# Kernel tuning notes

Measured on AMD Instinct MI355X. Metric: run time of the kernel, lower is better.

## Reference

```python
import jax, jax.numpy as jnp
import numpy as np

D_MODEL = 1024
NUM_HEADS = 16
HEAD_DIM = D_MODEL // NUM_HEADS
D_FF = 4 * D_MODEL


def _linear_params(key, d_in, d_out):
    kw, kb = jax.random.split(key)
    bound = 1.0 / np.sqrt(d_in)
    W = jax.random.uniform(kw, (d_in, d_out), minval=-bound, maxval=bound, dtype=jnp.float32)
    b = jax.random.uniform(kb, (d_out,), minval=-bound, maxval=bound, dtype=jnp.float32)
    return W, b


def setup_inputs() -> dict:
    key = jax.random.key(0)
    ks = jax.random.split(key, 6)
    x = jax.random.normal(ks[0], (4, 2048, D_MODEL), dtype=jnp.float32)
    qkv_w, qkv_b = _linear_params(ks[1], D_MODEL, 3 * D_MODEL)
    out_w, out_b = _linear_params(ks[2], D_MODEL, D_MODEL)
    ffn1_w, ffn1_b = _linear_params(ks[3], D_MODEL, D_FF)
    ffn2_w, ffn2_b = _linear_params(ks[4], D_FF, D_MODEL)
    ln1_g = jnp.ones((D_MODEL,), jnp.float32); ln1_b = jnp.zeros((D_MODEL,), jnp.float32)
    ln2_g = jnp.ones((D_MODEL,), jnp.float32); ln2_b = jnp.zeros((D_MODEL,), jnp.float32)
    return {
        "x": x,
        "qkv_w": qkv_w, "qkv_b": qkv_b,
        "out_w": out_w, "out_b": out_b,
        "ffn1_w": ffn1_w, "ffn1_b": ffn1_b,
        "ffn2_w": ffn2_w, "ffn2_b": ffn2_b,
        "ln1_g": ln1_g, "ln1_b": ln1_b,
        "ln2_g": ln2_g, "ln2_b": ln2_b,
    }


def _layer_norm(x, g, b, eps=1e-5):
    mu = jnp.mean(x, axis=-1, keepdims=True)
    var = jnp.mean(jnp.square(x - mu), axis=-1, keepdims=True)
    return (x - mu) * jax.lax.rsqrt(var + eps) * g + b


def reference(x, qkv_w, qkv_b, out_w, out_b, ffn1_w, ffn1_b, ffn2_w, ffn2_b,
              ln1_g, ln1_b, ln2_g, ln2_b):
    B, S, D = x.shape
    H, Hd = NUM_HEADS, HEAD_DIM
    normed = _layer_norm(x, ln1_g, ln1_b)
    qkv = normed @ qkv_w + qkv_b                      # [B,S,3D]
    qkv = qkv.reshape(B, S, 3, H, Hd)
    q = jnp.transpose(qkv[:, :, 0], (0, 2, 1, 3))     # [B,H,S,Hd]
    k = jnp.transpose(qkv[:, :, 1], (0, 2, 1, 3))
    v = jnp.transpose(qkv[:, :, 2], (0, 2, 1, 3))
    scores = jnp.einsum('bhqd,bhkd->bhqk', q, k) / np.sqrt(Hd).astype(np.float32)
    causal = jnp.tril(jnp.ones((S, S), dtype=bool))
    scores = jnp.where(causal[None, None], scores, -jnp.inf)
    attn = jax.nn.softmax(scores, axis=-1)
    attn_out = jnp.einsum('bhqk,bhkd->bhqd', attn, v)  # [B,H,S,Hd]
    attn_out = jnp.transpose(attn_out, (0, 2, 1, 3)).reshape(B, S, D)
    attn_out = attn_out @ out_w + out_b
    x = x + attn_out
    h = _layer_norm(x, ln2_g, ln2_b)
    h = jax.nn.gelu(h @ ffn1_w + ffn1_b, approximate=False)
    h = h @ ffn2_w + ffn2_b
    return x + h
```

## Files before the change

### kernel.cpp

```cpp
#include <hip/hip_runtime.h>
#include <hip/hip_bf16.h>
#include <math.h>

typedef __attribute__((ext_vector_type(8))) short short8;
typedef __attribute__((ext_vector_type(4))) float f32x4;

__device__ __forceinline__ float bf2f(unsigned short u) {
    union { unsigned int i; float f; } c; c.i = ((unsigned int)u) << 16; return c.f;
}
__device__ __forceinline__ unsigned short f2bf(float f) {
    union { float f; unsigned int i; } c; c.f = f;
    unsigned int i = c.i;
    unsigned int r = (i + 0x7FFFu + ((i >> 16) & 1u)) >> 16;
    return (unsigned short)r;
}
__device__ __forceinline__ float fexp2(float x) { return __builtin_amdgcn_exp2f(x); }

__device__ __forceinline__ void load8(const unsigned short* p, float* v) {
    short8 s = *(const short8*)p;
#pragma unroll
    for (int i = 0; i < 8; i++) v[i] = bf2f((unsigned short)s[i]);
}
__device__ __forceinline__ void load8(const float* p, float* v) {
    f32x4 a = ((const f32x4*)p)[0], b = ((const f32x4*)p)[1];
    v[0] = a[0]; v[1] = a[1]; v[2] = a[2]; v[3] = a[3];
    v[4] = b[0]; v[5] = b[1]; v[6] = b[2]; v[7] = b[3];
}
__device__ __forceinline__ void store8(unsigned short* p, const float* v) {
    short8 s;
#pragma unroll
    for (int i = 0; i < 8; i++) s[i] = (short)f2bf(v[i]);
    *(short8*)p = s;
}
__device__ __forceinline__ void store8(float* p, const float* v) {
    f32x4 a, b;
    a[0] = v[0]; a[1] = v[1]; a[2] = v[2]; a[3] = v[3];
    b[0] = v[4]; b[1] = v[5]; b[2] = v[6]; b[3] = v[7];
    ((f32x4*)p)[0] = a; ((f32x4*)p)[1] = b;
}

__global__ __launch_bounds__(256) void ln_f32_kernel(
    const float* __restrict__ x, const float* __restrict__ g,
    const float* __restrict__ b, unsigned short* __restrict__ out) {
    const int row = blockIdx.x;
    const int t = threadIdx.x;
    const float* xr = x + (size_t)row * 1024;
    float4 raw = ((const float4*)xr)[t];
    float v0 = raw.x, v1 = raw.y, v2 = raw.z, v3 = raw.w;
    float s = v0 + v1 + v2 + v3;
    float ss = v0 * v0 + v1 * v1 + v2 * v2 + v3 * v3;
    for (int off = 32; off > 0; off >>= 1) {
        s += __shfl_down(s, off);
        ss += __shfl_down(ss, off);
    }
    __shared__ float red[8];
    __shared__ float stat[2];
    const int wave = t >> 6, lane = t & 63;
    if (lane == 0) { red[wave] = s; red[4 + wave] = ss; }
    __syncthreads();
    if (t == 0) {
        float st = red[0] + red[1] + red[2] + red[3];
        float sst = red[4] + red[5] + red[6] + red[7];
        float mu = st * (1.0f / 1024.0f);
        float var = sst * (1.0f / 1024.0f) - mu * mu;
        stat[0] = mu; stat[1] = rsqrtf(var + 1e-5f);
    }
    __syncthreads();
    const float mu = stat[0], rstd = stat[1];
    float4 gr = ((const float4*)g)[t];
    float4 br = ((const float4*)b)[t];
    ushort4 o;
    o.x = f2bf((v0 - mu) * rstd * gr.x + br.x);
    o.y = f2bf((v1 - mu) * rstd * gr.y + br.y);
    o.z = f2bf((v2 - mu) * rstd * gr.z + br.z);
    o.w = f2bf((v3 - mu) * rstd * gr.w + br.w);
    ((ushort4*)(out + (size_t)row * 1024))[t] = o;
}

__global__ __launch_bounds__(256) void ln_bf16_kernel(
    const unsigned short* __restrict__ x, const float* __restrict__ g,
    const float* __restrict__ b, unsigned short* __restrict__ out) {
    const int row = blockIdx.x;
    const int t = threadIdx.x;
    const unsigned short* xr = x + (size_t)row * 1024;
    ushort4 raw = ((const ushort4*)xr)[t];
    float v0 = bf2f(raw.x), v1 = bf2f(raw.y), v2 = bf2f(raw.z), v3 = bf2f(raw.w);
    float s = v0 + v1 + v2 + v3;
    float ss = v0 * v0 + v1 * v1 + v2 * v2 + v3 * v3;
    for (int off = 32; off > 0; off >>= 1) {
        s += __shfl_down(s, off);
        ss += __shfl_down(ss, off);
    }
    __shared__ float red[8];
    __shared__ float stat[2];
    const int wave = t >> 6, lane = t & 63;
    if (lane == 0) { red[wave] = s; red[4 + wave] = ss; }
    __syncthreads();
    if (t == 0) {
        float st = red[0] + red[1] + red[2] + red[3];
        float sst = red[4] + red[5] + red[6] + red[7];
        float mu = st * (1.0f / 1024.0f);
        float var = sst * (1.0f / 1024.0f) - mu * mu;
        stat[0] = mu; stat[1] = rsqrtf(var + 1e-5f);
    }
    __syncthreads();
    const float mu = stat[0], rstd = stat[1];
    float4 gr = ((const float4*)g)[t];
    float4 br = ((const float4*)b)[t];
    ushort4 o;
    o.x = f2bf((v0 - mu) * rstd * gr.x + br.x);
    o.y = f2bf((v1 - mu) * rstd * gr.y + br.y);
    o.z = f2bf((v2 - mu) * rstd * gr.z + br.z);
    o.w = f2bf((v3 - mu) * rstd * gr.w + br.w);
    ((ushort4*)(out + (size_t)row * 1024))[t] = o;
}

__global__ __launch_bounds__(256) void transpose_cast_kernel(
    const float* __restrict__ in, unsigned short* __restrict__ out, int R, int C) {
    __shared__ unsigned short tile[32][33];
    const int bx = blockIdx.x * 32, by = blockIdx.y * 32;
    const int tx = threadIdx.x & 31, ty = threadIdx.x >> 5;
    for (int i = 0; i < 32; i += 8)
        tile[ty + i][tx] = f2bf(in[(size_t)(by + ty + i) * C + bx + tx]);
    __syncthreads();
    for (int i = 0; i < 32; i += 8)
        out[(size_t)(bx + ty + i) * R + by + tx] = tile[tx][ty + i];
}

enum { EPI_QKV = 0, EPI_RES = 1, EPI_GELU = 2 };

template <int EPI, typename RT, typename OT>
__global__ __launch_bounds__(256) void gemm_bt(
    const unsigned short* __restrict__ A, const unsigned short* __restrict__ Bt,
    const float* __restrict__ bias, const RT* __restrict__ res,
    OT* __restrict__ o0, unsigned short* __restrict__ o1,
    unsigned short* __restrict__ o2, int M, int N, int K) {
    constexpr int LDW = 40;
    constexpr int LE = 136;
    __shared__ __align__(16) unsigned short SMEM[20480];
    const int t = threadIdx.x;
    const int wave = t >> 6, lane = t & 63;
    const int lr = lane & 15, lq = lane >> 4;
    const int wm = (wave >> 1) * 64, wn = (wave & 1) * 64;
    const int m0 = blockIdx.y * 128, n0 = blockIdx.x * 128;
    f32x4 acc[4][4] = {};
    const int arow = t >> 2, acol = (t & 3) << 3;
    const unsigned short* ag = A + (size_t)(m0 + arow) * K + acol;
    const unsigned short* bg = Bt + (size_t)(n0 + arow) * K + acol;
    const size_t rstride = (size_t)64 * K;
    short8 a0 = *(const short8*)(ag);
    short8 a1 = *(const short8*)(ag + rstride);
    short8 b0 = *(const short8*)(bg);
    short8 b1 = *(const short8*)(bg + rstride);
    const int nit = K >> 5;
    for (int it = 0; it < nit; ++it) {
        const int buf = (it & 1) * 10240;
        unsigned short* As = SMEM + buf;
        unsigned short* Bs = SMEM + buf + 5120;
        *(short8*)(As + arow * LDW + acol) = a0;
        *(short8*)(As + (arow + 64) * LDW + acol) = a1;
        *(short8*)(Bs + arow * LDW + acol) = b0;
        *(short8*)(Bs + (arow + 64) * LDW + acol) = b1;
        if (it + 1 < nit) {
            const int k0 = (it + 1) << 5;
            a0 = *(const short8*)(ag + k0);
            a1 = *(const short8*)(ag + rstride + k0);
            b0 = *(const short8*)(bg + k0);
            b1 = *(const short8*)(bg + rstride + k0);
        }
        __syncthreads();
        short8 af[4], bfr[4];
#pragma unroll
        for (int i = 0; i < 4; i++) af[i] = *(const short8*)(As + (wm + i * 16 + lr) * LDW + lq * 8);
#pragma unroll
        for (int i = 0; i < 4; i++) bfr[i] = *(const short8*)(Bs + (wn + i * 16 + lr) * LDW + lq * 8);
#pragma unroll
        for (int mi = 0; mi < 4; mi++)
#pragma unroll
            for (int ni = 0; ni < 4; ni++)
                acc[mi][ni] = __builtin_amdgcn_mfma_f32_16x16x32_bf16(af[mi], bfr[ni], acc[mi][ni], 0, 0, 0);
    }
    __syncthreads();
    const bool vreg = (EPI == EPI_QKV) && (n0 >= 2048);
#pragma unroll
    for (int ni = 0; ni < 4; ni++) {
        const int col = wn + ni * 16 + lr;
        const float bv = bias[n0 + col];
#pragma unroll
        for (int mi = 0; mi < 4; mi++) {
#pragma unroll
            for (int r = 0; r < 4; r++) {
                const int row = wm + mi * 16 + lq * 4 + r;
                float val = acc[mi][ni][r] + bv;
                if (EPI == EPI_GELU)
                    val = 0.5f * val * (1.0f + erff(val * 0.70710678118654752f));
                if (vreg) SMEM[col * LE + row] = f2bf(val);
                else      SMEM[row * LE + col] = f2bf(val);
            }
        }
    }
    __syncthreads();
    const int rr = t >> 1, half = (t & 1) * 64;
    if (EPI == EPI_RES || EPI == EPI_GELU) {
        const size_t base = (size_t)(m0 + rr) * N + n0 + half;
        const unsigned short* src = SMEM + rr * LE + half;
#pragma unroll
        for (int j = 0; j < 8; j++) {
            float v[8];
            load8(src + j * 8, v);
            if (EPI == EPI_RES) {
                float rv[8];
                load8(res + base + j * 8, rv);
#pragma unroll
                for (int i = 0; i < 8; i++) v[i] += rv[i];
            }
            store8(o0 + base + j * 8, v);
        }
    } else if (!vreg) {
        const int gcol0 = n0 + half;
        const int which = gcol0 >> 10;
        const int hn = (gcol0 & 1023) >> 6;
        const int grow = m0 + rr;
        const size_t bh = (size_t)((grow >> 11) * 16 + hn);
        unsigned short* dst = (which == 0) ? (unsigned short*)o0 : o1;
        dst += (bh * 2048 + (grow & 2047)) * 64;
        const unsigned short* src = SMEM + rr * LE + half;
#pragma unroll
        for (int j = 0; j < 8; j++)
            *(short8*)(dst + j * 8) = *(const short8*)(src + j * 8);
    } else {
        const int c = rr;
        const int rem = (n0 + c) - 2048;
        const int hn = rem >> 6, d = rem & 63;
        const size_t bh = (size_t)((m0 >> 11) * 16 + hn);
        unsigned short* dst = o2 + (bh * 64 + d) * 2048 + (m0 & 2047) + half;
        const unsigned short* src = SMEM + c * LE + half;
#pragma unroll
        for (int j = 0; j < 8; j++)
            *(short8*)(dst + j * 8) = *(const short8*)(src + j * 8);
    }
}

__global__ __launch_bounds__(512) void attn_kernel(
    const unsigned short* __restrict__ qb, const unsigned short* __restrict__ kb,
    const unsigned short* __restrict__ vtb, unsigned short* __restrict__ aout) {
    const int bx = blockIdx.x;
    const int bh = blockIdx.y;
    const int bidx = bh >> 4, h = bh & 15;
    const int t = threadIdx.x, wave = t >> 6, lane = t & 63;
    const int lr = lane & 15, lq = lane >> 4;
    __shared__ __align__(16) unsigned short Ks[64 * 68];
    __shared__ __align__(16) unsigned short Vs[64 * 68];
    __shared__ __align__(16) unsigned short Ps[8][32 * 68];
    const unsigned short* kbase = kb + (size_t)bh * 2048 * 64;
    const unsigned short* vbase = vtb + (size_t)bh * 64 * 2048;
    const int srow = t >> 3, scol = (t & 7) * 8;
    const float kQScale = 0.125f * 1.44269504088896f;

    for (int phase = 0; phase < 2; phase++) {
        const int qblk = phase ? (7 - bx) : bx;
        const unsigned short* qbase = qb + ((size_t)bh * 2048 + qblk * 256 + wave * 32) * 64;
        short8 qf[2][2];
#pragma unroll
        for (int f = 0; f < 2; f++)
#pragma unroll
            for (int c = 0; c < 2; c++) {
                short8 raw = *(const short8*)(qbase + (f * 16 + lr) * 64 + c * 32 + lq * 8);
                short8 sc;
#pragma unroll
                for (int j = 0; j < 8; j++)
                    sc[j] = (short)f2bf(bf2f((unsigned short)raw[j]) * kQScale);
                qf[f][c] = sc;
            }
        f32x4 acc[2][4] = {};
        float m_i[2][4], l_i[2][4];
#pragma unroll
        for (int f = 0; f < 2; f++)
#pragma unroll
            for (int r = 0; r < 4; r++) { m_i[f][r] = -1e30f; l_i[f][r] = 0.0f; }
        const int wave_q0 = qblk * 256 + wave * 32;
        const int nkt = 4 * (qblk + 1);
        short8 kr = *(const short8*)(kbase + t * 8);
        short8 vr = *(const short8*)(vbase + (size_t)srow * 2048 + scol);
        for (int kt = 0; kt < nkt; kt++) {
            __syncthreads();
            *(short8*)(Ks + srow * 68 + scol) = kr;
            *(short8*)(Vs + srow * 68 + scol) = vr;
            __syncthreads();
            if (kt + 1 < nkt) {
                kr = *(const short8*)(kbase + (size_t)(kt + 1) * 4096 + t * 8);
                vr = *(const short8*)(vbase + (size_t)srow * 2048 + (kt + 1) * 64 + scol);
            }
            if (kt * 64 <= wave_q0 + 31) {
                f32x4 sa[2][4];
#pragma unroll
                for (int ni = 0; ni < 4; ni++) {
                    short8 kf0 = *(const short8*)(Ks + (ni * 16 + lr) * 68 + lq * 8);
                    short8 kf1 = *(const short8*)(Ks + (ni * 16 + lr) * 68 + 32 + lq * 8);
#pragma unroll
                    for (int f = 0; f < 2; f++) {
                        f32x4 z = {};
                        z = __builtin_amdgcn_mfma_f32_16x16x32_bf16(qf[f][0], kf0, z, 0, 0, 0);
                        sa[f][ni] = __builtin_amdgcn_mfma_f32_16x16x32_bf16(qf[f][1], kf1, z, 0, 0, 0);
                    }
                }
                const bool needmask = (kt * 64 + 63 > wave_q0);
                if (needmask) {
#pragma unroll
                    for (int f = 0; f < 2; f++) {
                        const int qrow0 = wave_q0 + f * 16 + lq * 4;
#pragma unroll
                        for (int ni = 0; ni < 4; ni++) {
                            const int kcol = kt * 64 + ni * 16 + lr;
#pragma unroll
                            for (int r = 0; r < 4; r++)
                                if (kcol > qrow0 + r) sa[f][ni][r] = -1e30f;
                        }
                    }
                }
#pragma unroll
                for (int f = 0; f < 2; f++) {
                    float mcur[4], alpha[4], rsum[4];
#pragma unroll
                    for (int r = 0; r < 4; r++)
                        mcur[r] = fmaxf(fmaxf(sa[f][0][r], sa[f][1][r]), fmaxf(sa[f][2][r], sa[f][3][r]));
#pragma unroll
                    for (int r = 0; r < 4; r++) {
#pragma unroll
                        for (int off = 1; off < 16; off <<= 1) mcur[r] = fmaxf(mcur[r], __shfl_xor(mcur[r], off));
                        const float mn = fmaxf(m_i[f][r], mcur[r]);
                        alpha[r] = fexp2(m_i[f][r] - mn);
                        m_i[f][r] = mn;
                        rsum[r] = 0.0f;
                    }
#pragma unroll
                    for (int ni = 0; ni < 4; ni++)
#pragma unroll
                        for (int r = 0; r < 4; r++) {
                            const float p = fexp2(sa[f][ni][r] - m_i[f][r]);
                            Ps[wave][(f * 16 + lq * 4 + r) * 68 + ni * 16 + lr] = f2bf(p);
                            rsum[r] += p;
                        }
#pragma unroll
                    for (int r = 0; r < 4; r++) {
#pragma unroll
                        for (int off = 1; off < 16; off <<= 1) rsum[r] += __shfl_xor(rsum[r], off);
                        l_i[f][r] = l_i[f][r] * alpha[r] + rsum[r];
#pragma unroll
                        for (int ni = 0; ni < 4; ni++) acc[f][ni][r] *= alpha[r];
                    }
                }
                short8 pf[2][2];
#pragma unroll
                for (int f = 0; f < 2; f++)
#pragma unroll
                    for (int c = 0; c < 2; c++)
                        pf[f][c] = *(const short8*)(&Ps[wave][(f * 16 + lr) * 68 + c * 32 + lq * 8]);
#pragma unroll
                for (int ni = 0; ni < 4; ni++) {
                    short8 vf0 = *(const short8*)(Vs + (ni * 16 + lr) * 68 + lq * 8);
                    short8 vf1 = *(const short8*)(Vs + (ni * 16 + lr) * 68 + 32 + lq * 8);
#pragma unroll
                    for (int f = 0; f < 2; f++) {
                        acc[f][ni] = __builtin_amdgcn_mfma_f32_16x16x32_bf16(pf[f][0], vf0, acc[f][ni], 0, 0, 0);
                        acc[f][ni] = __builtin_amdgcn_mfma_f32_16x16x32_bf16(pf[f][1], vf1, acc[f][ni], 0, 0, 0);
                    }
                }
            }
        }
#pragma unroll
        for (int f = 0; f < 2; f++)
#pragma unroll
            for (int r = 0; r < 4; r++) {
                const float rinv = 1.0f / l_i[f][r];
                const int q = qblk * 256 + wave * 32 + f * 16 + lq * 4 + r;
                const size_t token = (size_t)bidx * 2048 + q;
#pragma unroll
                for (int ni = 0; ni < 4; ni++)
                    aout[token * 1024 + h * 64 + ni * 16 + lr] = f2bf(acc[f][ni][r] * rinv);
            }
    }
}

extern "C" void kernel_launch(void* const* d_in, const int* in_sizes, int n_in,
                              void* d_out, int out_size, void* d_ws, size_t ws_size,
                              hipStream_t stream) {
    const float* x      = (const float*)d_in[0];
    const float* qkv_w  = (const float*)d_in[1];
    const float* qkv_b  = (const float*)d_in[2];
    const float* out_w  = (const float*)d_in[3];
    const float* out_b  = (const float*)d_in[4];
    const float* ffn1_w = (const float*)d_in[5];
    const float* ffn1_b = (const float*)d_in[6];
    const float* ffn2_w = (const float*)d_in[7];
    const float* ffn2_b = (const float*)d_in[8];
    const float* ln1_g  = (const float*)d_in[9];
    const float* ln1_b  = (const float*)d_in[10];
    const float* ln2_g  = (const float*)d_in[11];
    const float* ln2_b  = (const float*)d_in[12];
    float* out = (float*)d_out;
    char* W = (char*)d_ws;

    unsigned short* normed = (unsigned short*)(W);
    unsigned short* x1     = (unsigned short*)(W + 16777216);
    unsigned short* qbuf   = (unsigned short*)(W + 33554432);
    unsigned short* kbuf   = (unsigned short*)(W + 50331648);
    unsigned short* vbuf   = (unsigned short*)(W + 67108864);
    unsigned short* attnb  = (unsigned short*)(W + 83886080);
    unsigned short* hff    = (unsigned short*)(W + 33554432);
    unsigned short* qkv_wt = (unsigned short*)(W + 100663296);
    unsigned short* out_wt = (unsigned short*)(W + 106954752);
    unsigned short* f1_wt  = (unsigned short*)(W + 109051904);
    unsigned short* f2_wt  = (unsigned short*)(W + 117440512);

    transpose_cast_kernel<<<dim3(3072 / 32, 1024 / 32), 256, 0, stream>>>(qkv_w, qkv_wt, 1024, 3072);
    transpose_cast_kernel<<<dim3(1024 / 32, 1024 / 32), 256, 0, stream>>>(out_w, out_wt, 1024, 1024);
    transpose_cast_kernel<<<dim3(4096 / 32, 1024 / 32), 256, 0, stream>>>(ffn1_w, f1_wt, 1024, 4096);
    transpose_cast_kernel<<<dim3(1024 / 32, 4096 / 32), 256, 0, stream>>>(ffn2_w, f2_wt, 4096, 1024);

    ln_f32_kernel<<<dim3(8192), 256, 0, stream>>>(x, ln1_g, ln1_b, normed);
    gemm_bt<EPI_QKV, float, unsigned short><<<dim3(3072 / 128, 8192 / 128), 256, 0, stream>>>(
        normed, qkv_wt, qkv_b, nullptr, qbuf, kbuf, vbuf, 8192, 3072, 1024);
    attn_kernel<<<dim3(4, 64), 512, 0, stream>>>(qbuf, kbuf, vbuf, attnb);
    gemm_bt<EPI_RES, float, unsigned short><<<dim3(1024 / 128, 8192 / 128), 256, 0, stream>>>(
        attnb, out_wt, out_b, x, x1, nullptr, nullptr, 8192, 1024, 1024);
    ln_bf16_kernel<<<dim3(8192), 256, 0, stream>>>(x1, ln2_g, ln2_b, normed);
    gemm_bt<EPI_GELU, float, unsigned short><<<dim3(4096 / 128, 8192 / 128), 256, 0, stream>>>(
        normed, f1_wt, ffn1_b, nullptr, hff, nullptr, nullptr, 8192, 4096, 1024);
    gemm_bt<EPI_RES, unsigned short, float><<<dim3(1024 / 128, 8192 / 128), 256, 0, stream>>>(
        hff, f2_wt, ffn2_b, x1, out, nullptr, nullptr, 8192, 1024, 4096);
}
```

Baseline: 591.2 us.

## Add 256-row GEMM kernel with direct-to-LDS loads for FFN layers

Introduces a new 512-thread GEMM kernel with 256xBN tiles, double-buffered shared memory filled via global_load_lds, XOR-swizzled LDS layout, and a quadrant-interleaved MFMA schedule. It is used for both FFN GEMMs in place of the 128x128 kernel. The goal is more operand reuse per tile, less register staging of global loads, and overlap of loads with MFMA work. The cost is much more shared memory and register use per block, which may limit occupancy. The FFN2 launch has only 256 blocks, which may underfill the GPU.

After: 598.3 us. Within noise of the previous version (+1.2%).

```diff
diff --git a/kernel.cpp b/kernel.cpp
--- a/kernel.cpp
+++ b/kernel.cpp
@@ -15,6 +15,12 @@
     return (unsigned short)r;
 }
 __device__ __forceinline__ float fexp2(float x) { return __builtin_amdgcn_exp2f(x); }
+
+__device__ __forceinline__ void gload16(const unsigned short* g, unsigned short* l) {
+    __builtin_amdgcn_global_load_lds(
+        (const __attribute__((address_space(1))) unsigned int*)g,
+        (__attribute__((address_space(3))) unsigned int*)l, 16, 0, 0);
+}
 
 __device__ __forceinline__ void load8(const unsigned short* p, float* v) {
     short8 s = *(const short8*)p;
@@ -241,6 +247,160 @@
     }
 }
 
+template <int BN, int EPI, typename RT, typename OT>
+__global__ __launch_bounds__(512, 2) void gemm256(
+    const unsigned short* __restrict__ A, const unsigned short* __restrict__ Bt,
+    const float* __restrict__ bias, const RT* __restrict__ res,
+    OT* __restrict__ o0, unsigned short* __restrict__ o1,
+    unsigned short* __restrict__ o2, int M, int N, int K) {
+    constexpr int NFRAG = BN / 64;
+    constexpr int NF2 = NFRAG / 2;
+    constexpr int BQ = BN / 64;
+    constexpr int ASZ = 16384;
+    constexpr int BSZ = BN * 64;
+    constexpr int BUFSH = ASZ + BSZ;
+    constexpr int PE = BN + 8;
+    __shared__ __align__(16) unsigned short SMEM[2 * BUFSH];
+    const int t = threadIdx.x;
+    const int wave = t >> 6, lane = t & 63;
+    const int lr = lane & 15, lq = lane >> 4;
+    const int wm = wave >> 2, wn = wave & 3;
+    const int m0 = blockIdx.y * 256, n0 = blockIdx.x * BN;
+    const int xr3 = lr & 7;
+    f32x4 acc[8][NFRAG] = {};
+    short8 a[4][2], b0[NF2][2], b1[NF2][2];
+    const int srow = t >> 3;
+    const int scol = (((t & 7) ^ ((t >> 3) & 7)) << 3);
+    const unsigned short* agS = A + (size_t)(m0 + srow) * K + scol;
+    const unsigned short* bgS = Bt + (size_t)(n0 + srow) * K + scol;
+    const size_t q64K = (size_t)64 * K;
+
+#define STAGE_A(ktv, dv) do {                                                 \
+    unsigned short* dA_ = SMEM + (dv) * BUFSH;                                \
+    const int ko_ = (ktv) << 6;                                               \
+    _Pragma("unroll") for (int qi = 0; qi < 4; ++qi)                          \
+        gload16(agS + (size_t)qi * q64K + ko_, dA_ + qi * 4096 + t * 8);      \
+} while (0)
+
+#define STAGE_B(ktv, dv) do {                                                 \
+    unsigned short* dB_ = SMEM + (dv) * BUFSH + ASZ;                          \
+    const int ko_ = (ktv) << 6;                                               \
+    _Pragma("unroll") for (int qi = 0; qi < BQ; ++qi)                         \
+        gload16(bgS + (size_t)qi * q64K + ko_, dB_ + qi * 4096 + t * 8);      \
+} while (0)
+
+#define READ_A(qm) do {                                                       \
+    _Pragma("unroll") for (int mi = 0; mi < 4; ++mi) {                        \
+        const int rA_ = wm * 128 + (qm) * 64 + mi * 16 + lr;                  \
+        _Pragma("unroll") for (int ks = 0; ks < 2; ++ks)                      \
+            a[mi][ks] = *(const short8*)(Ash + rA_ * 64 + (((ks * 4 + lq) ^ xr3) << 3)); \
+    } } while (0)
+
+#define READ_B(qn, barr) do {                                                 \
+    _Pragma("unroll") for (int ni = 0; ni < NF2; ++ni) {                      \
+        const int rB_ = wn * (BN / 4) + (qn) * (BN / 8) + ni * 16 + lr;       \
+        _Pragma("unroll") for (int ks = 0; ks < 2; ++ks)                      \
+            barr[ni][ks] = *(const short8*)(Bsh + rB_ * 64 + (((ks * 4 + lq) ^ xr3) << 3)); \
+    } } while (0)
+
+#define MFMAQ(qm, qn, barr) do {                                              \
+    _Pragma("unroll") for (int mi = 0; mi < 4; ++mi)                          \
+        _Pragma("unroll") for (int ni = 0; ni < NF2; ++ni) {                  \
+            f32x4 c_ = acc[(qm) * 4 + mi][(qn) * NF2 + ni];                   \
+            c_ = __builtin_amdgcn_mfma_f32_16x16x32_bf16(a[mi][0], barr[ni][0], c_, 0, 0, 0); \
+            c_ = __builtin_amdgcn_mfma_f32_16x16x32_bf16(a[mi][1], barr[ni][1], c_, 0, 0, 0); \
+            acc[(qm) * 4 + mi][(qn) * NF2 + ni] = c_;                         \
+        } } while (0)
+
+#define BARRIER __builtin_amdgcn_s_barrier()
+#define VMW4 asm volatile("s_waitcnt vmcnt(4)" ::: "memory")
+#define VMW0 asm volatile("s_waitcnt vmcnt(0)" ::: "memory")
+
+    const int nkt = K >> 6;
+    STAGE_A(0, 0);
+    STAGE_B(0, 0);
+    if (nkt > 1) { STAGE_A(1, 1); VMW4; } else { VMW0; }
+    BARRIER;
+    for (int kt = 0; kt < nkt; ++kt) {
+        const unsigned short* Ash = SMEM + (kt & 1) * BUFSH;
+        const unsigned short* Bsh = Ash + ASZ;
+        READ_A(0);
+        READ_B(0, b0);
+        if (kt + 1 < nkt) STAGE_B(kt + 1, (kt + 1) & 1);
+        BARRIER;
+        MFMAQ(0, 0, b0);
+        BARRIER;
+        READ_B(1, b1);
+        BARRIER;
+        MFMAQ(0, 1, b1);
+        BARRIER;
+        READ_A(1);
+        BARRIER;
+        MFMAQ(1, 1, b1);
+        BARRIER;
+        if (kt + 2 < nkt) {
+            STAGE_A(kt + 2, kt & 1);
+            MFMAQ(1, 0, b0);
+            VMW4;
+        } else {
+            MFMAQ(1, 0, b0);
+            VMW0;
+        }
+        BARRIER;
+    }
+#undef STAGE_A
+#undef STAGE_B
+#undef READ_A
+#undef READ_B
+#undef MFMAQ
+#undef BARRIER
+#undef VMW4
+#undef VMW0
+
+    __syncthreads();
+    const bool vreg = (EPI == EPI_QKV) && (n0 >= 2048);
+    for (int h = 0; h < 2; ++h) {
+        if (h) __syncthreads();
+        if (wm == h) {
+#pragma unroll
+            for (int nj = 0; nj < NFRAG; ++nj) {
+                const int col = wn * (BN / 4) + nj * 16 + lr;
+                const float bv = bias[n0 + col];
+#pragma unroll
+                for (int mi = 0; mi < 8; ++mi) {
+#pragma unroll
+                    for (int r = 0; r < 4; ++r) {
+                        const int lrow = mi * 16 + lq * 4 + r;
+                        float val = acc[mi][nj][r] + bv;
+                        if (EPI == EPI_GELU)
+                            val = 0.5f * val * (1.0f + erff(val * 0.70710678118654752f));
+                        if (vreg) SMEM[col * 136 + lrow] = f2bf(val);
+                        else      SMEM[lrow * PE + col] = f2bf(val);
+                    }
+                }
+            }
+        }
+        __syncthreads();
+        if (EPI == EPI_RES || EPI == EPI_GELU) {
+            const int rr = t >> 2, sg = (t & 3) * (BN / 4);
+            const size_t base = (size_t)(m0 + h * 128 + rr) * N + n0 + sg;
+            const unsigned short* src = SMEM + rr * PE + sg;
+#pragma unroll
+            for (int j = 0; j < BN / 32; ++j) {
+                float v[8];
+                load8(src + j * 8, v);
+                if (EPI == EPI_RES) {
+                    float rv[8];
+                    load8(res + base + j * 8, rv);
+#pragma unroll
+                    for (int i = 0; i < 8; i++) v[i] += rv[i];
+                }
+                store8(o0 + base + j * 8, v);
+            }
+        }
+    }
+}
+
 __global__ __launch_bounds__(512) void attn_kernel(
     const unsigned short* __restrict__ qb, const unsigned short* __restrict__ kb,
     const unsigned short* __restrict__ vtb, unsigned short* __restrict__ aout) {
@@ -425,8 +585,8 @@
     gemm_bt<EPI_RES, float, unsigned short><<<dim3(1024 / 128, 8192 / 128), 256, 0, stream>>>(
         attnb, out_wt, out_b, x, x1, nullptr, nullptr, 8192, 1024, 1024);
     ln_bf16_kernel<<<dim3(8192), 256, 0, stream>>>(x1, ln2_g, ln2_b, normed);
-    gemm_bt<EPI_GELU, float, unsigned short><<<dim3(4096 / 128, 8192 / 128), 256, 0, stream>>>(
+    gemm256<256, EPI_GELU, float, unsigned short><<<dim3(4096 / 256, 8192 / 256), 512, 0, stream>>>(
         normed, f1_wt, ffn1_b, nullptr, hff, nullptr, nullptr, 8192, 4096, 1024);
-    gemm_bt<EPI_RES, unsigned short, float><<<dim3(1024 / 128, 8192 / 128), 256, 0, stream>>>(
+    gemm256<128, EPI_RES, unsigned short, float><<<dim3(1024 / 128, 8192 / 256), 512, 0, stream>>>(
         hff, f2_wt, ffn2_b, x1, out, nullptr, nullptr, 8192, 1024, 4096);
 }
```
